# Kernel optimization log

Measured on AMD Instinct MI355X. Metric: run time of the kernel, lower is better.

The kernel has to match this reference:

```python
import jax, jax.numpy as jnp
import numpy as np
import math

H = 8  # num_heads

def setup_inputs() -> dict:
    key = jax.random.key(0)
    ks = jax.random.split(key, 12)
    B, N, M, k = 2, 8192, 8192, 32
    dq, dk, dv = 256, 256, 256
    s = 1.0 / math.sqrt(dq)
    inp = {
        'Q': jax.random.normal(ks[0], (B, N, dq), dtype=jnp.float32),
        'K': jax.random.normal(ks[1], (B, M, dk), dtype=jnp.float32),
        'neighbours': jax.random.randint(ks[2], (B, N, k), 0, M),
        'Wq': jax.random.normal(ks[3], (dq, dv), dtype=jnp.float32) * s,
        'bq': jnp.zeros((dv,), dtype=jnp.float32),
        'Wk': jax.random.normal(ks[4], (dk, dv), dtype=jnp.float32) * s,
        'bk': jnp.zeros((dv,), dtype=jnp.float32),
        'Wv': jax.random.normal(ks[5], (dk, dv), dtype=jnp.float32) * s,
        'bv': jnp.zeros((dv,), dtype=jnp.float32),
        'Wo': jax.random.normal(ks[6], (dv, dv), dtype=jnp.float32) * (1.0 / math.sqrt(dv)),
        'bo': jnp.zeros((dv,), dtype=jnp.float32),
    }
    return inp

def reference(Q, K, neighbours, Wq, bq, Wk, bk, Wv, bv, Wo, bo):
    B, N, _ = Q.shape
    dv = Wq.shape[1]
    ds = dv // H
    # project and split heads (contiguous channel chunks == reshape)
    Qh = (Q @ Wq + bq).reshape(B, N, H, ds)            # [B,N,H,ds]
    Kh = (K @ Wk + bk).reshape(B, -1, H, ds)           # [B,M,H,ds]
    Vh = (K @ Wv + bv).reshape(B, -1, H, ds)           # [B,M,H,ds]
    # gather per-node kNN neighbour keys/values: [B,N,k,H,ds]
    gather = jax.vmap(lambda x, idx: x[idx])
    Kn = gather(Kh, neighbours)
    Vn = gather(Vh, neighbours)
    # scale uses full latent size (faithful to original), not head dim
    scale = 1.0 / math.sqrt(dv)
    E = jnp.einsum('bnhd,bnkhd->bnhk', Qh, Kn) * scale  # [B,N,H,k]
    A = jax.nn.softmax(E, axis=-1)
    AV = jnp.einsum('bnhk,bnkhd->bnhd', A, Vn).reshape(B, N, dv)
    return AV @ Wo + bo
```

## Files before the change

kernel.cpp:

```cpp
#include <hip/hip_runtime.h>
#include <hip/hip_bf16.h>
#include <stdint.h>

typedef unsigned short u16;
typedef __attribute__((ext_vector_type(8))) short short8;
typedef __attribute__((ext_vector_type(4))) float f32x4;

__device__ __forceinline__ u16 f2bf(float f) {
    union { float f; unsigned int i; } v; v.f = f;
    unsigned int b = v.i;
    return (u16)((b + 0x7FFFu + ((b >> 16) & 1u)) >> 16);
}

__device__ __forceinline__ short8 cvt8(float4 a, float4 b) {
    union { __hip_bfloat162 h[4]; short8 s; } u;
    u.h[0] = __float22bfloat162_rn(make_float2(a.x, a.y));
    u.h[1] = __float22bfloat162_rn(make_float2(a.z, a.w));
    u.h[2] = __float22bfloat162_rn(make_float2(b.x, b.y));
    u.h[3] = __float22bfloat162_rn(make_float2(b.z, b.w));
    return u.s;
}

typedef const __attribute__((address_space(1))) void* as1cv;
typedef __attribute__((address_space(3))) void* as3v;
__device__ __forceinline__ void gload16(const void* g, void* l) {
    __builtin_amdgcn_global_load_lds((as1cv)g, (as3v)l, 16, 0, 0);
}

__device__ __forceinline__ void up2(unsigned int v, float& lo, float& hi) {
    union { unsigned int i; float f; } a, b;
    a.i = v << 16; b.i = v & 0xffff0000u;
    lo = a.f; hi = b.f;
}

__global__ __launch_bounds__(256) void wprep(
    const float* __restrict__ W0, const float* __restrict__ W1,
    const float* __restrict__ W2, const float* __restrict__ W3,
    u16* __restrict__ T0, u16* __restrict__ T1,
    u16* __restrict__ T2, u16* __restrict__ T3)
{
    const float* W = blockIdx.z == 0 ? W0 : blockIdx.z == 1 ? W1 : blockIdx.z == 2 ? W2 : W3;
    u16*        T  = blockIdx.z == 0 ? T0 : blockIdx.z == 1 ? T1 : blockIdx.z == 2 ? T2 : T3;
    __shared__ u16 ts[64][65];
    int k0 = blockIdx.x * 64, n0 = blockIdx.y * 64;
    int t = threadIdx.x;
    int r = t >> 2, cq = (t & 3) * 16;
    const float4* src = reinterpret_cast<const float4*>(W + (k0 + r) * 256 + n0 + cq);
    for (int u = 0; u < 4; ++u) {
        float4 v = src[u];
        int c = cq + u * 4;
        ts[r][c + 0] = f2bf(v.x); ts[r][c + 1] = f2bf(v.y);
        ts[r][c + 2] = f2bf(v.z); ts[r][c + 3] = f2bf(v.w);
    }
    __syncthreads();
    u16* dst = T + (n0 + r) * 256 + k0 + cq;
    for (int u = 0; u < 16; ++u) dst[u] = ts[cq + u][r];
}

__global__ __launch_bounds__(256) void gemm_proj(
    const float* __restrict__ Q, const float* __restrict__ K,
    const u16* __restrict__ Wtq, const u16* __restrict__ Wtk, const u16* __restrict__ Wtv,
    const float* __restrict__ bq, const float* __restrict__ bk, const float* __restrict__ bv,
    u16* __restrict__ Qh, u16* __restrict__ Kh, u16* __restrict__ Vh)
{
    int z = blockIdx.z;
    const float* Af   = (z == 0) ? Q   : K;
    const u16*   Wt   = (z == 0) ? Wtq : (z == 1) ? Wtk : Wtv;
    const float* bias = (z == 0) ? bq  : (z == 1) ? bk  : bv;
    u16*         C    = (z == 0) ? Qh  : (z == 1) ? Kh  : Vh;

    __shared__ float Asf[64 * 64];
    __shared__ u16   Bs[256 * 64];

    int t = threadIdx.x;
    int lane = t & 63, w = t >> 6;
    int row0 = blockIdx.x * 64;
    int wr = (w >> 1) * 32, wc = (w & 1) * 128;
    int qd = lane >> 4, md = lane & 15;

    f32x4 acc[2][8] = {};

    for (int kt = 0; kt < 256; kt += 64) {
#pragma unroll
        for (int u = 0; u < 4; ++u) {
            int chunk = w * 4 + u;
            int s = chunk * 64 + lane;
            int r = s >> 4, c = s & 15;
            gload16(Af + (size_t)(row0 + r) * 256 + kt + ((c ^ (r & 15)) * 4),
                    (char*)Asf + chunk * 1024);
        }
#pragma unroll
        for (int u = 0; u < 8; ++u) {
            int chunk = w * 8 + u;
            int s = chunk * 64 + lane;
            int r = s >> 3, c = s & 7;
            gload16(Wt + (size_t)r * 256 + kt + ((c ^ (r & 7)) * 8),
                    (char*)Bs + chunk * 1024);
        }
        __syncthreads();
#pragma unroll
        for (int ks = 0; ks < 64; ks += 32) {
            short8 af[2], bf[8];
#pragma unroll
            for (int i = 0; i < 2; ++i) {
                int ar = wr + i * 16 + md;
                int c0 = (ks >> 2) + qd * 2;
                int xx = ar & 15;
                float4 fa0 = reinterpret_cast<const float4*>(Asf)[ar * 16 + (c0 ^ xx)];
                float4 fa1 = reinterpret_cast<const float4*>(Asf)[ar * 16 + ((c0 + 1) ^ xx)];
                af[i] = cvt8(fa0, fa1);
            }
#pragma unroll
            for (int j = 0; j < 8; ++j) {
                int br = wc + j * 16 + md;
                int slot = ((ks >> 3) + qd) ^ (br & 7);
                bf[j] = reinterpret_cast<const short8*>(Bs)[br * 8 + slot];
            }
#pragma unroll
            for (int i = 0; i < 2; ++i)
#pragma unroll
                for (int j = 0; j < 8; ++j)
                    acc[i][j] = __builtin_amdgcn_mfma_f32_16x16x32_bf16(
                        af[i], bf[j], acc[i][j], 0, 0, 0);
        }
        __syncthreads();
    }

#pragma unroll
    for (int i = 0; i < 2; ++i)
#pragma unroll
        for (int j = 0; j < 8; ++j) {
            int col = wc + j * 16 + md;
            float b = bias[col];
#pragma unroll
            for (int r = 0; r < 4; ++r) {
                int row = row0 + wr + i * 16 + qd * 4 + r;
                C[(size_t)row * 256 + col] = f2bf(acc[i][j][r] + b);
            }
        }
}

__global__ __launch_bounds__(256) void gemm_out(
    const u16* __restrict__ Ab, const u16* __restrict__ Wt,
    const float* __restrict__ bias, float* __restrict__ Cout)
{
    __shared__ u16 As[64 * 64];
    __shared__ u16 Bs[128 * 64];

    int t = threadIdx.x;
    int lane = t & 63, w = t >> 6;
    int row0 = blockIdx.x * 64, col0 = blockIdx.y * 128;
    int wr = (w >> 1) * 32, wc = (w & 1) * 64;
    int qd = lane >> 4, md = lane & 15;

    f32x4 acc[2][4] = {};

    for (int kt = 0; kt < 256; kt += 64) {
#pragma unroll
        for (int u = 0; u < 2; ++u) {
            int chunk = w * 2 + u;
            int s = chunk * 64 + lane;
            int r = s >> 3, c = s & 7;
            gload16(Ab + (size_t)(row0 + r) * 256 + kt + ((c ^ (r & 7)) * 8),
                    (char*)As + chunk * 1024);
        }
#pragma unroll
        for (int u = 0; u < 4; ++u) {
            int chunk = w * 4 + u;
            int s = chunk * 64 + lane;
            int r = s >> 3, c = s & 7;
            gload16(Wt + (size_t)(col0 + r) * 256 + kt + ((c ^ (r & 7)) * 8),
                    (char*)Bs + chunk * 1024);
        }
        __syncthreads();
#pragma unroll
        for (int ks = 0; ks < 64; ks += 32) {
            short8 af[2], bf[4];
#pragma unroll
            for (int i = 0; i < 2; ++i) {
                int ar = wr + i * 16 + md;
                int slot = ((ks >> 3) + qd) ^ (ar & 7);
                af[i] = reinterpret_cast<const short8*>(As)[ar * 8 + slot];
            }
#pragma unroll
            for (int j = 0; j < 4; ++j) {
                int br = wc + j * 16 + md;
                int slot = ((ks >> 3) + qd) ^ (br & 7);
                bf[j] = reinterpret_cast<const short8*>(Bs)[br * 8 + slot];
            }
#pragma unroll
            for (int i = 0; i < 2; ++i)
#pragma unroll
                for (int j = 0; j < 4; ++j)
                    acc[i][j] = __builtin_amdgcn_mfma_f32_16x16x32_bf16(
                        af[i], bf[j], acc[i][j], 0, 0, 0);
        }
        __syncthreads();
    }

#pragma unroll
    for (int i = 0; i < 2; ++i)
#pragma unroll
        for (int j = 0; j < 4; ++j) {
            int col = col0 + wc + j * 16 + md;
            float b = bias[col];
#pragma unroll
            for (int r = 0; r < 4; ++r) {
                int row = row0 + wr + i * 16 + qd * 4 + r;
                Cout[(size_t)row * 256 + col] = acc[i][j][r] + b;
            }
        }
}

__device__ __forceinline__ void attn_map2(int blk, int w, int& row, int& hf) {
    int g = blk & 7;
    int batch = g >> 2;
    hf = (g >> 1) & 1;
    int cb = (blk >> 3) * 2 + (g & 1);
    row = batch * 8192 + cb * 4 + w;
}

__global__ __launch_bounds__(256) void attn_fused(
    const u16* __restrict__ Qh, const u16* __restrict__ Kh,
    const u16* __restrict__ Vh, const int* __restrict__ nbr,
    u16* __restrict__ AVb)
{
    __shared__ int jbs[4][32];

    int t = threadIdx.x;
    int w = t >> 6, lane = t & 63;
    int blk2 = blockIdx.x & 8191;
    int row, hf;
    attn_map2(blk2, w, row, hf);
    int bbase = (row >> 13) << 13;

    int c4 = lane & 15;
    int jg = lane >> 4;

    if (lane < 32) {
        int ji = nbr[(size_t)row * 32 + lane];
        jbs[w][lane] = (bbase + ji) * 256 + hf * 128;
    }

    float qf[8];
    {
        uint4 qw = *reinterpret_cast<const uint4*>(Qh + (size_t)row * 256 + hf * 128 + c4 * 8);
        up2(qw.x, qf[0], qf[1]); up2(qw.y, qf[2], qf[3]);
        up2(qw.z, qf[4], qf[5]); up2(qw.w, qf[6], qf[7]);
    }

    int off[8];
#pragma unroll
    for (int u = 0; u < 8; ++u) off[u] = jbs[w][jg * 8 + u];

    uint4 kw[8];
#pragma unroll
    for (int u = 0; u < 8; ++u)
        kw[u] = *reinterpret_cast<const uint4*>(Kh + (size_t)off[u] + c4 * 8);

    uint4 vv[8];
#pragma unroll
    for (int u = 0; u < 8; ++u)
        vv[u] = *reinterpret_cast<const uint4*>(Vh + (size_t)off[u] + c4 * 8);

    float e8[8];
#pragma unroll
    for (int u = 0; u < 8; ++u) {
        float k0, k1;
        float p = 0.f;
        up2(kw[u].x, k0, k1); p = fmaf(qf[0], k0, p); p = fmaf(qf[1], k1, p);
        up2(kw[u].y, k0, k1); p = fmaf(qf[2], k0, p); p = fmaf(qf[3], k1, p);
        up2(kw[u].z, k0, k1); p = fmaf(qf[4], k0, p); p = fmaf(qf[5], k1, p);
        up2(kw[u].w, k0, k1); p = fmaf(qf[6], k0, p); p = fmaf(qf[7], k1, p);
        p += __shfl_xor(p, 1);
        p += __shfl_xor(p, 2);
        e8[u] = p * 0.0625f;
    }

    float m = e8[0];
#pragma unroll
    for (int jj = 1; jj < 8; ++jj) m = fmaxf(m, e8[jj]);
    m = fmaxf(m, __shfl_xor(m, 16));
    m = fmaxf(m, __shfl_xor(m, 32));
    float s = 0.f;
#pragma unroll
    for (int jj = 0; jj < 8; ++jj) { e8[jj] = __expf(e8[jj] - m); s += e8[jj]; }
    s += __shfl_xor(s, 16);
    s += __shfl_xor(s, 32);
    float rs = 1.0f / s;

    float acc[8] = {};
#pragma unroll
    for (int u = 0; u < 8; ++u) {
        float v0, v1;
        float wgt = e8[u] * rs;
        up2(vv[u].x, v0, v1); acc[0] = fmaf(wgt, v0, acc[0]); acc[1] = fmaf(wgt, v1, acc[1]);
        up2(vv[u].y, v0, v1); acc[2] = fmaf(wgt, v0, acc[2]); acc[3] = fmaf(wgt, v1, acc[3]);
        up2(vv[u].z, v0, v1); acc[4] = fmaf(wgt, v0, acc[4]); acc[5] = fmaf(wgt, v1, acc[5]);
        up2(vv[u].w, v0, v1); acc[6] = fmaf(wgt, v0, acc[6]); acc[7] = fmaf(wgt, v1, acc[7]);
    }
#pragma unroll
    for (int u = 0; u < 8; ++u) {
        acc[u] += __shfl_xor(acc[u], 16);
        acc[u] += __shfl_xor(acc[u], 32);
    }

    if (lane < 16) {
        union { __hip_bfloat162 h2[4]; uint4 u4; } o;
        o.h2[0] = __float22bfloat162_rn(make_float2(acc[0], acc[1]));
        o.h2[1] = __float22bfloat162_rn(make_float2(acc[2], acc[3]));
        o.h2[2] = __float22bfloat162_rn(make_float2(acc[4], acc[5]));
        o.h2[3] = __float22bfloat162_rn(make_float2(acc[6], acc[7]));
        *reinterpret_cast<uint4*>(AVb + (size_t)row * 256 + hf * 128 + c4 * 8) = o.u4;
    }
}

extern "C" void kernel_launch(void* const* d_in, const int* in_sizes, int n_in,
                              void* d_out, int out_size, void* d_ws, size_t ws_size,
                              hipStream_t stream) {
    const float* Q   = (const float*)d_in[0];
    const float* K   = (const float*)d_in[1];
    const int*   nbr = (const int*)d_in[2];
    const float* Wq  = (const float*)d_in[3];
    const float* bq  = (const float*)d_in[4];
    const float* Wk  = (const float*)d_in[5];
    const float* bk  = (const float*)d_in[6];
    const float* Wv  = (const float*)d_in[7];
    const float* bv  = (const float*)d_in[8];
    const float* Wo  = (const float*)d_in[9];
    const float* bo  = (const float*)d_in[10];
    float* out = (float*)d_out;

    char* ws = (char*)d_ws;
    size_t off = 0;
    auto alloc = [&](size_t bytes) -> void* {
        void* p = ws + off;
        off += (bytes + 255) & ~(size_t)255;
        return p;
    };
    const size_t MN = 16384;
    u16* Wtq = (u16*)alloc(256 * 256 * 2);
    u16* Wtk = (u16*)alloc(256 * 256 * 2);
    u16* Wtv = (u16*)alloc(256 * 256 * 2);
    u16* Wto = (u16*)alloc(256 * 256 * 2);
    u16* Qh  = (u16*)alloc(MN * 256 * 2);
    u16* Kh  = (u16*)alloc(MN * 256 * 2);
    u16* Vh  = (u16*)alloc(MN * 256 * 2);
    u16* AVb = (u16*)alloc(MN * 256 * 2);

    wprep<<<dim3(4, 4, 4), 256, 0, stream>>>(Wq, Wk, Wv, Wo, Wtq, Wtk, Wtv, Wto);
    gemm_proj<<<dim3(256, 1, 3), 256, 0, stream>>>(Q, K, Wtq, Wtk, Wtv,
                                                   bq, bk, bv, Qh, Kh, Vh);
    attn_fused<<<dim3(16384), 256, 0, stream>>>(Qh, Kh, Vh, nbr, AVb);
    gemm_out<<<dim3(256, 2), 256, 0, stream>>>(AVb, Wto, bo, out);
}
```

Measured before the change: 169.3 us.

## Store projected K/V in fp32, use packed f32x2 math, halve attention grid

Measured after the change: 192.1 us. +13.5%, slower.

```diff
diff --git a/kernel.cpp b/kernel.cpp
--- a/kernel.cpp
+++ b/kernel.cpp
@@ -5,6 +5,7 @@
 typedef unsigned short u16;
 typedef __attribute__((ext_vector_type(8))) short short8;
 typedef __attribute__((ext_vector_type(4))) float f32x4;
+typedef __attribute__((ext_vector_type(2))) float f32x2;
 
 __device__ __forceinline__ u16 f2bf(float f) {
     union { float f; unsigned int i; } v; v.f = f;
@@ -61,13 +62,12 @@
     const float* __restrict__ Q, const float* __restrict__ K,
     const u16* __restrict__ Wtq, const u16* __restrict__ Wtk, const u16* __restrict__ Wtv,
     const float* __restrict__ bq, const float* __restrict__ bk, const float* __restrict__ bv,
-    u16* __restrict__ Qh, u16* __restrict__ Kh, u16* __restrict__ Vh)
+    u16* __restrict__ Qh, float* __restrict__ Khf, float* __restrict__ Vhf)
 {
     int z = blockIdx.z;
     const float* Af   = (z == 0) ? Q   : K;
     const u16*   Wt   = (z == 0) ? Wtq : (z == 1) ? Wtk : Wtv;
     const float* bias = (z == 0) ? bq  : (z == 1) ? bk  : bv;
-    u16*         C    = (z == 0) ? Qh  : (z == 1) ? Kh  : Vh;
 
     __shared__ float Asf[64 * 64];
     __shared__ u16   Bs[256 * 64];
@@ -135,7 +135,10 @@
 #pragma unroll
             for (int r = 0; r < 4; ++r) {
                 int row = row0 + wr + i * 16 + qd * 4 + r;
-                C[(size_t)row * 256 + col] = f2bf(acc[i][j][r] + b);
+                float v = acc[i][j][r] + b;
+                if (z == 0)      Qh [(size_t)row * 256 + col] = f2bf(v);
+                else if (z == 1) Khf[(size_t)row * 256 + col] = v;
+                else             Vhf[(size_t)row * 256 + col] = v;
             }
         }
 }
@@ -221,17 +224,16 @@
 }
 
 __global__ __launch_bounds__(256) void attn_fused(
-    const u16* __restrict__ Qh, const u16* __restrict__ Kh,
-    const u16* __restrict__ Vh, const int* __restrict__ nbr,
+    const u16* __restrict__ Qh, const float* __restrict__ Khf,
+    const float* __restrict__ Vhf, const int* __restrict__ nbr,
     u16* __restrict__ AVb)
 {
     __shared__ int jbs[4][32];
 
     int t = threadIdx.x;
     int w = t >> 6, lane = t & 63;
-    int blk2 = blockIdx.x & 8191;
     int row, hf;
-    attn_map2(blk2, w, row, hf);
+    attn_map2(blockIdx.x, w, row, hf);
     int bbase = (row >> 13) << 13;
 
     int c4 = lane & 15;
@@ -242,36 +244,33 @@
         jbs[w][lane] = (bbase + ji) * 256 + hf * 128;
     }
 
-    float qf[8];
+    f32x2 q2[4];
     {
         uint4 qw = *reinterpret_cast<const uint4*>(Qh + (size_t)row * 256 + hf * 128 + c4 * 8);
-        up2(qw.x, qf[0], qf[1]); up2(qw.y, qf[2], qf[3]);
-        up2(qw.z, qf[4], qf[5]); up2(qw.w, qf[6], qf[7]);
+        float qa[8];
+        up2(qw.x, qa[0], qa[1]); up2(qw.y, qa[2], qa[3]);
+        up2(qw.z, qa[4], qa[5]); up2(qw.w, qa[6], qa[7]);
+#pragma unroll
+        for (int j = 0; j < 4; ++j) { q2[j].x = qa[2 * j]; q2[j].y = qa[2 * j + 1]; }
     }
 
     int off[8];
 #pragma unroll
     for (int u = 0; u < 8; ++u) off[u] = jbs[w][jg * 8 + u];
 
-    uint4 kw[8];
-#pragma unroll
-    for (int u = 0; u < 8; ++u)
-        kw[u] = *reinterpret_cast<const uint4*>(Kh + (size_t)off[u] + c4 * 8);
-
-    uint4 vv[8];
-#pragma unroll
-    for (int u = 0; u < 8; ++u)
-        vv[u] = *reinterpret_cast<const uint4*>(Vh + (size_t)off[u] + c4 * 8);
-
     float e8[8];
 #pragma unroll
     for (int u = 0; u < 8; ++u) {
-        float k0, k1;
-        float p = 0.f;
-        up2(kw[u].x, k0, k1); p = fmaf(qf[0], k0, p); p = fmaf(qf[1], k1, p);
-        up2(kw[u].y, k0, k1); p = fmaf(qf[2], k0, p); p = fmaf(qf[3], k1, p);
-        up2(kw[u].z, k0, k1); p = fmaf(qf[4], k0, p); p = fmaf(qf[5], k1, p);
-        up2(kw[u].w, k0, k1); p = fmaf(qf[6], k0, p); p = fmaf(qf[7], k1, p);
+        const float4* kp = reinterpret_cast<const float4*>(Khf + (size_t)off[u] + c4 * 8);
+        float4 ka = kp[0], kb = kp[1];
+        f32x2 k0, k1, k2, k3;
+        k0.x = ka.x; k0.y = ka.y; k1.x = ka.z; k1.y = ka.w;
+        k2.x = kb.x; k2.y = kb.y; k3.x = kb.z; k3.y = kb.w;
+        f32x2 p2 = q2[0] * k0;
+        p2 += q2[1] * k1;
+        p2 += q2[2] * k2;
+        p2 += q2[3] * k3;
+        float p = p2.x + p2.y;
         p += __shfl_xor(p, 1);
         p += __shfl_xor(p, 2);
         e8[u] = p * 0.0625f;
@@ -289,16 +288,25 @@
     s += __shfl_xor(s, 32);
     float rs = 1.0f / s;
 
-    float acc[8] = {};
+    f32x2 a2[4] = {};
 #pragma unroll
     for (int u = 0; u < 8; ++u) {
-        float v0, v1;
+        const float4* vp = reinterpret_cast<const float4*>(Vhf + (size_t)off[u] + c4 * 8);
+        float4 va = vp[0], vb = vp[1];
         float wgt = e8[u] * rs;
-        up2(vv[u].x, v0, v1); acc[0] = fmaf(wgt, v0, acc[0]); acc[1] = fmaf(wgt, v1, acc[1]);
-        up2(vv[u].y, v0, v1); acc[2] = fmaf(wgt, v0, acc[2]); acc[3] = fmaf(wgt, v1, acc[3]);
-        up2(vv[u].z, v0, v1); acc[4] = fmaf(wgt, v0, acc[4]); acc[5] = fmaf(wgt, v1, acc[5]);
-        up2(vv[u].w, v0, v1); acc[6] = fmaf(wgt, v0, acc[6]); acc[7] = fmaf(wgt, v1, acc[7]);
-    }
+        f32x2 w2; w2.x = wgt; w2.y = wgt;
+        f32x2 v0, v1, v2, v3;
+        v0.x = va.x; v0.y = va.y; v1.x = va.z; v1.y = va.w;
+        v2.x = vb.x; v2.y = vb.y; v3.x = vb.z; v3.y = vb.w;
+        a2[0] += w2 * v0;
+        a2[1] += w2 * v1;
+        a2[2] += w2 * v2;
+        a2[3] += w2 * v3;
+    }
+
+    float acc[8];
+#pragma unroll
+    for (int j = 0; j < 4; ++j) { acc[2 * j] = a2[j].x; acc[2 * j + 1] = a2[j].y; }
 #pragma unroll
     for (int u = 0; u < 8; ++u) {
         acc[u] += __shfl_xor(acc[u], 16);
@@ -339,18 +347,18 @@
         return p;
     };
     const size_t MN = 16384;
-    u16* Wtq = (u16*)alloc(256 * 256 * 2);
-    u16* Wtk = (u16*)alloc(256 * 256 * 2);
-    u16* Wtv = (u16*)alloc(256 * 256 * 2);
-    u16* Wto = (u16*)alloc(256 * 256 * 2);
-    u16* Qh  = (u16*)alloc(MN * 256 * 2);
-    u16* Kh  = (u16*)alloc(MN * 256 * 2);
-    u16* Vh  = (u16*)alloc(MN * 256 * 2);
-    u16* AVb = (u16*)alloc(MN * 256 * 2);
+    u16*   Wtq = (u16*)alloc(256 * 256 * 2);
+    u16*   Wtk = (u16*)alloc(256 * 256 * 2);
+    u16*   Wtv = (u16*)alloc(256 * 256 * 2);
+    u16*   Wto = (u16*)alloc(256 * 256 * 2);
+    u16*   Qh  = (u16*)alloc(MN * 256 * 2);
+    float* Khf = (float*)alloc(MN * 256 * 4);
+    float* Vhf = (float*)alloc(MN * 256 * 4);
+    u16*   AVb = (u16*)alloc(MN * 256 * 2);
 
     wprep<<<dim3(4, 4, 4), 256, 0, stream>>>(Wq, Wk, Wv, Wo, Wtq, Wtk, Wtv, Wto);
     gemm_proj<<<dim3(256, 1, 3), 256, 0, stream>>>(Q, K, Wtq, Wtk, Wtv,
-                                                   bq, bk, bv, Qh, Kh, Vh);
-    attn_fused<<<dim3(16384), 256, 0, stream>>>(Qh, Kh, Vh, nbr, AVb);
+                                                   bq, bk, bv, Qh, Khf, Vhf);
+    attn_fused<<<dim3(8192), 256, 0, stream>>>(Qh, Khf, Vhf, nbr, AVb);
     gemm_out<<<dim3(256, 2), 256, 0, stream>>>(AVb, Wto, bo, out);
 }
```
